# Performance work log

Measured on AMD Instinct MI355X. Metric: run time of the kernel, lower is better.

Reference implementation:

```python
import jax, jax.numpy as jnp
import numpy as np
from jax import lax

N_CLS = 4
ALPHA = 1.0
EPS = 1e-4


def _level_loss(logit, prob_gt, coord_gt, weight_cls):
    # logit: [B, N_cls*A, D, H, W]; prob_gt: [B, A, D, H, W]; coord_gt: [B, K, 4] int
    B, C, D, H, W = logit.shape
    A = C // N_CLS
    logit6 = logit.reshape(B, N_CLS, A, D, H, W)
    prob = jnp.clip(jax.nn.sigmoid(logit6), EPS, 1.0 - EPS)  # [B,N_cls,A,D,H,W]
    prob_max = jnp.max(prob, axis=1)                          # [B,A,D,H,W]

    # --- negative (background) focal term with NMS peak masking ---
    negmask = (prob_gt == -1.0).astype(logit.dtype)
    pooled = lax.reduce_window(prob_max, -jnp.inf, lax.max,
                               (1, 1, 3, 3, 3), (1, 1, 1, 1, 1),
                               [(0, 0), (0, 0), (1, 1), (1, 1), (1, 1)])
    max_filter = lax.stop_gradient((pooled == prob_max).astype(logit.dtype))
    thresh_filter = (prob_max > EPS).astype(logit.dtype)
    negmask = negmask * max_filter * thresh_filter
    w_neg = lax.stop_gradient(prob_max) ** ALPHA * negmask
    loss_neg = -jnp.sum(jnp.log(1.0 - prob_max) * w_neg)
    count_neg = jnp.sum(w_neg)

    # --- positive + other-class terms at sparse GT coordinates (vmapped over batch) ---
    def per_item(p_pred, l_pred, c_gt, p_gt):
        # p_pred/l_pred: [N_cls,A,D,H,W]; c_gt: [K,4]; p_gt: [A,D,H,W]
        valid = c_gt[:, 0] > -1
        vmask = valid.astype(p_pred.dtype)
        c = jnp.where(valid[:, None], c_gt, 0)  # safe indices for padded rows
        a, d, h, w = c[:, 0], c[:, 1], c[:, 2], c[:, 3]
        cls_gt = jnp.clip(p_gt[a, d, h, w].astype(jnp.int32) - 1, 0, N_CLS - 1)  # [K]
        p_t = p_pred[cls_gt, a, d, h, w]  # [K]
        l_t = l_pred[cls_gt, a, d, h, w]
        w_pos = (1.0 - lax.stop_gradient(p_t)) ** ALPHA * weight_cls[cls_gt] * vmask
        loss_pos = -jnp.sum(jax.nn.log_sigmoid(l_t) * w_pos)
        count_pos = jnp.sum(w_pos)
        # other-class suppression
        p_o = p_pred[:, a, d, h, w]  # [N_cls, K]
        l_o = l_pred[:, a, d, h, w]
        w_o = lax.stop_gradient(
            jax.nn.relu(p_o - (p_t - 0.05))
            * (p_o > 0.5).astype(p_o.dtype)
            * (p_t > 0.5).astype(p_o.dtype))
        # torch: weight[cls_gt] = 0  -> zero entire rows for classes present among valid GTs
        present = jnp.zeros((N_CLS,), p_pred.dtype).at[cls_gt].max(vmask)
        w_o = w_o * (1.0 - present)[:, None] * vmask[None, :]
        loss_other = jnp.sum(-jax.nn.log_sigmoid(-l_o) * w_o)
        count_other = jnp.sum(w_o)
        return loss_pos, count_pos, loss_other, count_other

    lp, cp, lo, co = jax.vmap(per_item)(prob, logit6, coord_gt, prob_gt)
    return (jnp.sum(lp), loss_neg, jnp.sum(lo), jnp.sum(cp), count_neg, jnp.sum(co))


def _forward(logits0, logits1, gtprob0, gtprob1, coords0, coords1, weight_cls):
    r0 = _level_loss(logits0, gtprob0, coords0, weight_cls)
    r1 = _level_loss(logits1, gtprob1, coords1, weight_cls)
    # [loss_pos, loss_neg, loss_other, count_pos, count_neg, count_other]
    return jnp.stack([a + b for a, b in zip(r0, r1)])


def setup_inputs() -> dict:
    rng = np.random.default_rng(0)
    B, A = 2, 2
    level_shapes = [(64, 128, 128), (32, 64, 64)]
    K, K_VALID = 32, 24
    out = {}
    for i, (D, H, W) in enumerate(level_shapes):
        logits = rng.standard_normal((B, N_CLS * A, D, H, W)).astype(np.float32)
        gt = -np.ones((B, A, D, H, W), np.float32)
        coords = -np.ones((B, K, 4), np.int32)
        for b in range(B):
            a = rng.integers(0, A, K_VALID)
            d = rng.integers(0, D, K_VALID)
            h = rng.integers(0, H, K_VALID)
            w = rng.integers(0, W, K_VALID)
            cls = rng.integers(1, N_CLS + 1, K_VALID)
            gt[b, a, d, h, w] = cls.astype(np.float32)
            coords[b, :K_VALID, 0] = a
            coords[b, :K_VALID, 1] = d
            coords[b, :K_VALID, 2] = h
            coords[b, :K_VALID, 3] = w
        out[f"logits{i}"] = jnp.asarray(logits)
        out[f"gtprob{i}"] = jnp.asarray(gt)
        out[f"coords{i}"] = jnp.asarray(coords)
    out["weight_cls"] = jnp.ones((N_CLS,), jnp.float32)
    return out


def reference(logits0, logits1, gtprob0, gtprob1, coords0, coords1, weight_cls):
    return _forward(logits0, logits1, gtprob0, gtprob1, coords0, coords1, weight_cls)
```

## Files before the change

kernel.cpp:

```cpp
#include <hip/hip_runtime.h>
#include <math.h>

#define EPSF 1e-4f
#define NBLK 1024

static __device__ __forceinline__ float sigmoid_fast(float x) {
    float e = __expf(-x);
    float p = __builtin_amdgcn_rcpf(1.0f + e);
    return fminf(fmaxf(p, EPSF), 1.0f - EPSF);
}
static __device__ __forceinline__ float sigmoid_precise(float x) {
    float p = 1.0f / (1.0f + expf(-x));
    return fminf(fmaxf(p, EPSF), 1.0f - EPSF);
}
static __device__ __forceinline__ float softplus(float x) {
    return fmaxf(x, 0.0f) + log1pf(expf(-fabsf(x)));
}
static __device__ __forceinline__ float4 fmax4(float4 a, float4 b) {
    float4 r;
    r.x = fmaxf(a.x, b.x); r.y = fmaxf(a.y, b.y);
    r.z = fmaxf(a.z, b.z); r.w = fmaxf(a.w, b.w);
    return r;
}
static __device__ __forceinline__ float4 sig4(float4 x) {
    float4 r;
    r.x = sigmoid_fast(x.x); r.y = sigmoid_fast(x.y);
    r.z = sigmoid_fast(x.z); r.w = sigmoid_fast(x.w);
    return r;
}

template <int WG, int Wc>
static __device__ __forceinline__ float4 wmax_row(const float* pm, int row, int w0) {
    const float4 v = *(const float4*)(pm + (size_t)row * Wc + 4 * w0);
    float lft = __shfl_up(v.w, 1);
    float rgt = __shfl_down(v.x, 1);
    lft = (w0 == 0) ? -INFINITY : lft;
    rgt = (w0 == WG - 1) ? -INFINITY : rgt;
    float4 r;
    r.x = fmaxf(fmaxf(lft, v.x), v.y);
    r.y = fmaxf(fmaxf(v.x, v.y), v.z);
    r.z = fmaxf(fmaxf(v.y, v.z), v.w);
    r.w = fmaxf(fmaxf(v.z, v.w), rgt);
    return r;
}
template <int WG, int Wc>
static __device__ __forceinline__ float4 hfold(const float* pm, int row0, int w0) {
    return fmax4(fmax4(wmax_row<WG, Wc>(pm, row0, w0), wmax_row<WG, Wc>(pm, row0 + 1, w0)),
                 wmax_row<WG, Wc>(pm, row0 + 2, w0));
}

template <int Wc, int TD, int TH>
static __device__ void neg_tile(const float* __restrict__ logits,
                                const float* __restrict__ gtprob,
                                int D, int H, int tileIdx, float* pm,
                                double& lsum, double& csum) {
    constexpr int WG = Wc / 4;
    constexpr int NROWH = TH + 2;
    constexpr int NROW = (TD + 2) * NROWH;
    constexpr int RPP = 512 / WG;
    constexpr int G = 512 / WG;
    const int ht = tileIdx & 15, dt = (tileIdx >> 4) & 15, ab = tileIdx >> 8;
    const int a = ab & 1, b = ab >> 1;
    const int h0 = ht * TH, d0 = dt * TD;
    size_t HW = (size_t)H * Wc;
    size_t vol = (size_t)D * HW;
    const float* lg = logits + ((size_t)b * 8 + a) * vol;
    const size_t cs = 2 * vol;
    const float* gtb = gtprob + ((size_t)b * 2 + a) * vol;
    const int tid = threadIdx.x;
    const int w0 = tid % WG, rg = tid / WG;

#pragma unroll
    for (int r = rg; r < NROW; r += RPP) {
        int rd = r / NROWH, rh = r - rd * NROWH;
        int d = d0 + rd - 1, h = h0 + rh - 1;
        float4 v = make_float4(-INFINITY, -INFINITY, -INFINITY, -INFINITY);
        if ((unsigned)d < (unsigned)D && (unsigned)h < (unsigned)H) {
            const float* p0 = lg + (size_t)d * HW + (size_t)h * Wc + 4 * w0;
            float4 c0 = *(const float4*)(p0);
            float4 c1 = *(const float4*)(p0 + cs);
            float4 c2 = *(const float4*)(p0 + 2 * cs);
            float4 c3 = *(const float4*)(p0 + 3 * cs);
            v = sig4(fmax4(fmax4(c0, c1), fmax4(c2, c3)));
        }
        *(float4*)(pm + (size_t)r * Wc + 4 * w0) = v;
    }
    __syncthreads();

    for (int cidx = rg; cidx < TD * TH; cidx += G) {
        int dd = cidx / TH, hh = cidx - dd * TH;
        float4 hm0 = hfold<WG, Wc>(pm, (dd + 0) * NROWH + hh, w0);
        float4 hm1 = hfold<WG, Wc>(pm, (dd + 1) * NROWH + hh, w0);
        float4 hm2 = hfold<WG, Wc>(pm, (dd + 2) * NROWH + hh, w0);
        float4 mx = fmax4(fmax4(hm0, hm1), hm2);
        float4 pc = *(const float4*)(pm + (size_t)((dd + 1) * NROWH + hh + 1) * Wc + 4 * w0);
        const float* gp = gtb + (size_t)(d0 + dd) * HW + (size_t)(h0 + hh) * Wc + 4 * w0;
        float4 g = *(const float4*)gp;
        if (g.x == -1.0f && mx.x == pc.x && pc.x > EPSF) {
            lsum += (double)(-__logf(1.0f - pc.x) * pc.x); csum += (double)pc.x;
        }
        if (g.y == -1.0f && mx.y == pc.y && pc.y > EPSF) {
            lsum += (double)(-__logf(1.0f - pc.y) * pc.y); csum += (double)pc.y;
        }
        if (g.z == -1.0f && mx.z == pc.z && pc.z > EPSF) {
            lsum += (double)(-__logf(1.0f - pc.z) * pc.z); csum += (double)pc.z;
        }
        if (g.w == -1.0f && mx.w == pc.w && pc.w > EPSF) {
            lsum += (double)(-__logf(1.0f - pc.w) * pc.w); csum += (double)pc.w;
        }
    }
}

__global__ __launch_bounds__(512) void fused_kernel(
    const float* __restrict__ lg0, const float* __restrict__ gt0, const int* __restrict__ c0,
    const float* __restrict__ lg1, const float* __restrict__ gt1, const int* __restrict__ c1,
    const float* __restrict__ wcls, double* __restrict__ slots,
    unsigned* __restrict__ counter, float* __restrict__ out) {
    __shared__ float pm[60 * 128];
    __shared__ double spart[48];
    __shared__ unsigned present[4];
    __shared__ bool isLast;
    int tid = threadIdx.x;
    int bid = blockIdx.x;
    double v0 = 0, v1 = 0, v2 = 0, v3 = 0, v4 = 0, v5 = 0;

    if (bid == 0) {
        if (tid < 4) present[tid] = 0u;
        __syncthreads();
        int lvl = (tid >> 6) & 1, tt = tid & 63;
        int b = tt >> 5, k = tt & 31;
        const float* lg = lvl ? lg1 : lg0;
        const float* gt = lvl ? gt1 : gt0;
        const int* cd = lvl ? c1 : c0;
        int D = lvl ? 32 : 64, H = lvl ? 64 : 128, Wd = lvl ? 64 : 128;
        int a = 0, d = 0, h = 0, w = 0, cls = 0;
        bool valid = false;
        size_t vol = (size_t)D * H * Wd, off = 0;
        if (tid < 128) {
            const int* c = cd + ((size_t)b * 32 + k) * 4;
            a = c[0]; d = c[1]; h = c[2]; w = c[3];
            valid = a > -1;
            if (!valid) { a = 0; d = 0; h = 0; w = 0; }
            off = ((size_t)d * H + h) * (size_t)Wd + w;
            float gval = gt[((size_t)b * 2 + a) * vol + off];
            cls = (int)gval - 1;
            cls = cls < 0 ? 0 : (cls > 3 ? 3 : cls);
            if (valid) atomicOr(&present[lvl * 2 + b], 1u << cls);
        }
        __syncthreads();
        if (tid < 128) {
            unsigned pmask = present[lvl * 2 + b];
            float vm = valid ? 1.0f : 0.0f;
            const float* lgb = lg + (size_t)b * 8 * vol;
            size_t aoff = (size_t)a * vol + off;
            float l_t = lgb[(size_t)cls * 2 * vol + aoff];
            float p_t = sigmoid_precise(l_t);
            float w_pos = (1.0f - p_t) * wcls[cls] * vm;
            float loss_pos = softplus(-l_t) * w_pos;
            float ptg = (p_t > 0.5f) ? 1.0f : 0.0f;
            float lo = 0.0f, co = 0.0f;
#pragma unroll
            for (int cc = 0; cc < 4; cc++) {
                float l_o = lgb[(size_t)cc * 2 * vol + aoff];
                float p_o = sigmoid_precise(l_o);
                float wo = fmaxf(p_o - (p_t - 0.05f), 0.0f) * ((p_o > 0.5f) ? 1.0f : 0.0f) * ptg;
                float pres = ((pmask >> cc) & 1u) ? 1.0f : 0.0f;
                wo *= (1.0f - pres) * vm;
                lo += softplus(l_o) * wo;
                co += wo;
            }
            v0 = loss_pos; v3 = w_pos; v2 = lo; v5 = co;
        }
        __syncthreads();
    }

    neg_tile<128, 4, 8>(lg0, gt0, 64, 128, bid, pm, v1, v4);
    __syncthreads();
    neg_tile<64, 2, 4>(lg1, gt1, 32, 64, bid, pm, v1, v4);

    for (int o = 32; o > 0; o >>= 1) {
        v0 += __shfl_down(v0, o); v1 += __shfl_down(v1, o); v2 += __shfl_down(v2, o);
        v3 += __shfl_down(v3, o); v4 += __shfl_down(v4, o); v5 += __shfl_down(v5, o);
    }
    int wave = tid >> 6, lane = tid & 63;
    if (lane == 0) {
        double* sp = spart + wave * 6;
        sp[0] = v0; sp[1] = v1; sp[2] = v2; sp[3] = v3; sp[4] = v4; sp[5] = v5;
    }
    __syncthreads();
    if (tid == 0) {
        double s[6] = {0, 0, 0, 0, 0, 0};
#pragma unroll
        for (int wv = 0; wv < 8; wv++)
#pragma unroll
            for (int j = 0; j < 6; j++) s[j] += spart[wv * 6 + j];
        double* slot = slots + (size_t)bid * 6;
#pragma unroll
        for (int j = 0; j < 6; j++) slot[j] = s[j];
        __threadfence();
        unsigned prev = atomicAdd(counter, 1u);
        isLast = (prev == NBLK - 1);
    }
    __syncthreads();
    if (isLast) {
        __threadfence();
        double acc[6] = {0, 0, 0, 0, 0, 0};
        for (int i = tid; i < NBLK; i += 512) {
            const double* sl = slots + (size_t)i * 6;
#pragma unroll
            for (int j = 0; j < 6; j++) acc[j] += sl[j];
        }
#pragma unroll
        for (int j = 0; j < 6; j++)
            for (int o = 32; o > 0; o >>= 1) acc[j] += __shfl_down(acc[j], o);
        __syncthreads();
        if (lane == 0) {
            double* sp = spart + wave * 6;
#pragma unroll
            for (int j = 0; j < 6; j++) sp[j] = acc[j];
        }
        __syncthreads();
        if (tid == 0) {
#pragma unroll
            for (int j = 0; j < 6; j++) {
                double s = 0;
#pragma unroll
                for (int wv = 0; wv < 8; wv++) s += spart[wv * 6 + j];
                out[j] = (float)s;
            }
        }
    }
}

extern "C" void kernel_launch(void* const* d_in, const int* in_sizes, int n_in,
                              void* d_out, int out_size, void* d_ws, size_t ws_size,
                              hipStream_t stream) {
    const float *logits0 = nullptr, *gtprob0 = nullptr, *logits1 = nullptr,
                *gtprob1 = nullptr, *wcls = nullptr;
    const int *coords0 = nullptr, *coords1 = nullptr;
    for (int i = 0; i < n_in; i++) {
        switch (in_sizes[i]) {
            case 16777216: logits0 = (const float*)d_in[i]; break;
            case 4194304:  gtprob0 = (const float*)d_in[i]; break;
            case 2097152:  logits1 = (const float*)d_in[i]; break;
            case 524288:   gtprob1 = (const float*)d_in[i]; break;
            case 4:        wcls    = (const float*)d_in[i]; break;
            case 256:
                if (!coords0) coords0 = (const int*)d_in[i];
                else          coords1 = (const int*)d_in[i];
                break;
        }
    }
    unsigned* counter = (unsigned*)d_ws;
    double* slots = (double*)((char*)d_ws + 64);
    hipMemsetAsync(d_ws, 0, 64, stream);
    fused_kernel<<<NBLK, 512, 0, stream>>>(logits0, gtprob0, coords0,
                                           logits1, gtprob1, coords1,
                                           wcls, slots, counter, (float*)d_out);
}
```

Before: 163.7 us.

## Split levels across separate block ranges, prefetch rows, use global atomics

Each block now handles a single level's tile: 1024 blocks take level 0 and 128 blocks take level 1 with larger tiles, so a block no longer runs both levels back to back. The halo-row loader is software-pipelined, fetching the next row's four class loads before computing the current one, and ground-truth loads are hoisted ahead of the barrier. The last-block slot reduction is replaced with double atomicAdd into six global accumulators plus a tiny finalize kernel. This adds a second launch and double atomics, and makes the summation order nondeterministic.

```diff
diff --git a/kernel.cpp b/kernel.cpp
--- a/kernel.cpp
+++ b/kernel.cpp
@@ -2,7 +2,9 @@
 #include <math.h>
 
 #define EPSF 1e-4f
-#define NBLK 1024
+#define NB_L1 128
+#define NB_L0 1024
+#define NBLK (NB_L1 + NB_L0)
 
 static __device__ __forceinline__ float sigmoid_fast(float x) {
     float e = __expf(-x);
@@ -49,53 +51,90 @@
                  wmax_row<WG, Wc>(pm, row0 + 2, w0));
 }
 
-template <int Wc, int TD, int TH>
+template <int Wc, int TD, int TH, int D, int H>
 static __device__ void neg_tile(const float* __restrict__ logits,
                                 const float* __restrict__ gtprob,
-                                int D, int H, int tileIdx, float* pm,
+                                int tileIdx, float* pm,
                                 double& lsum, double& csum) {
     constexpr int WG = Wc / 4;
     constexpr int NROWH = TH + 2;
     constexpr int NROW = (TD + 2) * NROWH;
     constexpr int RPP = 512 / WG;
-    constexpr int G = 512 / WG;
-    const int ht = tileIdx & 15, dt = (tileIdx >> 4) & 15, ab = tileIdx >> 8;
+    constexpr int NPASS = (NROW + RPP - 1) / RPP;
+    constexpr int NCELL = TD * TH;
+    constexpr int CPT = (NCELL + RPP - 1) / RPP;
+    constexpr int NH = H / TH, ND = D / TD;
+    const int ht = tileIdx % NH;
+    const int dt = (tileIdx / NH) % ND;
+    const int ab = tileIdx / (NH * ND);
     const int a = ab & 1, b = ab >> 1;
     const int h0 = ht * TH, d0 = dt * TD;
-    size_t HW = (size_t)H * Wc;
-    size_t vol = (size_t)D * HW;
+    const size_t HW = (size_t)H * Wc;
+    const size_t vol = (size_t)D * HW;
     const float* lg = logits + ((size_t)b * 8 + a) * vol;
     const size_t cs = 2 * vol;
     const float* gtb = gtprob + ((size_t)b * 2 + a) * vol;
     const int tid = threadIdx.x;
     const int w0 = tid % WG, rg = tid / WG;
 
-#pragma unroll
-    for (int r = rg; r < NROW; r += RPP) {
-        int rd = r / NROWH, rh = r - rd * NROWH;
+    auto rowinfo = [&](int r, bool& inb) -> const float* {
+        int rc = r < NROW - 1 ? r : NROW - 1;
+        int rd = rc / NROWH, rh = rc - rd * NROWH;
         int d = d0 + rd - 1, h = h0 + rh - 1;
-        float4 v = make_float4(-INFINITY, -INFINITY, -INFINITY, -INFINITY);
-        if ((unsigned)d < (unsigned)D && (unsigned)h < (unsigned)H) {
-            const float* p0 = lg + (size_t)d * HW + (size_t)h * Wc + 4 * w0;
-            float4 c0 = *(const float4*)(p0);
-            float4 c1 = *(const float4*)(p0 + cs);
-            float4 c2 = *(const float4*)(p0 + 2 * cs);
-            float4 c3 = *(const float4*)(p0 + 3 * cs);
-            v = sig4(fmax4(fmax4(c0, c1), fmax4(c2, c3)));
-        }
-        *(float4*)(pm + (size_t)r * Wc + 4 * w0) = v;
+        inb = ((unsigned)d < (unsigned)D) & ((unsigned)h < (unsigned)H) & (r < NROW);
+        int dc = d < 0 ? 0 : (d >= D ? D - 1 : d);
+        int hc = h < 0 ? 0 : (h >= H ? H - 1 : h);
+        return lg + (size_t)dc * HW + (size_t)hc * Wc + 4 * w0;
+    };
+
+    float4 n0, n1, n2, n3;
+    bool ninb;
+    {
+        const float* p = rowinfo(rg, ninb);
+        n0 = *(const float4*)p;            n1 = *(const float4*)(p + cs);
+        n2 = *(const float4*)(p + 2 * cs); n3 = *(const float4*)(p + 3 * cs);
+    }
+#pragma unroll
+    for (int ps = 0; ps < NPASS; ps++) {
+        float4 c0 = n0, c1 = n1, c2 = n2, c3 = n3;
+        bool inb = ninb;
+        int r = rg + ps * RPP;
+        if (ps + 1 < NPASS) {
+            bool ib;
+            const float* q = rowinfo(rg + (ps + 1) * RPP, ib);
+            ninb = ib;
+            n0 = *(const float4*)q;            n1 = *(const float4*)(q + cs);
+            n2 = *(const float4*)(q + 2 * cs); n3 = *(const float4*)(q + 3 * cs);
+        }
+        float4 v = sig4(fmax4(fmax4(c0, c1), fmax4(c2, c3)));
+        if (!inb) v = make_float4(-INFINITY, -INFINITY, -INFINITY, -INFINITY);
+        if (r < NROW) *(float4*)(pm + (size_t)r * Wc + 4 * w0) = v;
+    }
+
+    float4 gq[CPT];
+    int cdd[CPT], chh[CPT];
+    bool cok[CPT];
+#pragma unroll
+    for (int k = 0; k < CPT; k++) {
+        int cidx = rg + k * RPP;
+        bool ok = cidx < NCELL;
+        int ci = ok ? cidx : 0;
+        int dd = ci / TH, hh = ci - dd * TH;
+        cdd[k] = dd; chh[k] = hh; cok[k] = ok;
+        gq[k] = *(const float4*)(gtb + (size_t)(d0 + dd) * HW + (size_t)(h0 + hh) * Wc + 4 * w0);
     }
     __syncthreads();
 
-    for (int cidx = rg; cidx < TD * TH; cidx += G) {
-        int dd = cidx / TH, hh = cidx - dd * TH;
+#pragma unroll
+    for (int k = 0; k < CPT; k++) {
+        if (!cok[k]) continue;
+        int dd = cdd[k], hh = chh[k];
         float4 hm0 = hfold<WG, Wc>(pm, (dd + 0) * NROWH + hh, w0);
         float4 hm1 = hfold<WG, Wc>(pm, (dd + 1) * NROWH + hh, w0);
         float4 hm2 = hfold<WG, Wc>(pm, (dd + 2) * NROWH + hh, w0);
         float4 mx = fmax4(fmax4(hm0, hm1), hm2);
         float4 pc = *(const float4*)(pm + (size_t)((dd + 1) * NROWH + hh + 1) * Wc + 4 * w0);
-        const float* gp = gtb + (size_t)(d0 + dd) * HW + (size_t)(h0 + hh) * Wc + 4 * w0;
-        float4 g = *(const float4*)gp;
+        float4 g = gq[k];
         if (g.x == -1.0f && mx.x == pc.x && pc.x > EPSF) {
             lsum += (double)(-__logf(1.0f - pc.x) * pc.x); csum += (double)pc.x;
         }
@@ -114,73 +153,78 @@
 __global__ __launch_bounds__(512) void fused_kernel(
     const float* __restrict__ lg0, const float* __restrict__ gt0, const int* __restrict__ c0,
     const float* __restrict__ lg1, const float* __restrict__ gt1, const int* __restrict__ c1,
-    const float* __restrict__ wcls, double* __restrict__ slots,
-    unsigned* __restrict__ counter, float* __restrict__ out) {
+    const float* __restrict__ wcls, double* __restrict__ gacc) {
     __shared__ float pm[60 * 128];
     __shared__ double spart[48];
     __shared__ unsigned present[4];
-    __shared__ bool isLast;
     int tid = threadIdx.x;
     int bid = blockIdx.x;
     double v0 = 0, v1 = 0, v2 = 0, v3 = 0, v4 = 0, v5 = 0;
 
+    if (bid >= NB_L1) {
+        neg_tile<128, 4, 8, 64, 128>(lg0, gt0, bid - NB_L1, pm, v1, v4);
+    } else {
+        if (bid == 0) {
+            if (tid < 4) present[tid] = 0u;
+            __syncthreads();
+            int lvl = (tid >> 6) & 1, tt = tid & 63;
+            int b = tt >> 5, k = tt & 31;
+            const float* lg = lvl ? lg1 : lg0;
+            const float* gt = lvl ? gt1 : gt0;
+            const int* cd = lvl ? c1 : c0;
+            int D = lvl ? 32 : 64, H = lvl ? 64 : 128, Wd = lvl ? 64 : 128;
+            int a = 0, d = 0, h = 0, w = 0, cls = 0;
+            bool valid = false;
+            size_t vol = (size_t)D * H * Wd, off = 0;
+            if (tid < 128) {
+                const int* c = cd + ((size_t)b * 32 + k) * 4;
+                a = c[0]; d = c[1]; h = c[2]; w = c[3];
+                valid = a > -1;
+                if (!valid) { a = 0; d = 0; h = 0; w = 0; }
+                off = ((size_t)d * H + h) * (size_t)Wd + w;
+                float gval = gt[((size_t)b * 2 + a) * vol + off];
+                cls = (int)gval - 1;
+                cls = cls < 0 ? 0 : (cls > 3 ? 3 : cls);
+                if (valid) atomicOr(&present[lvl * 2 + b], 1u << cls);
+            }
+            __syncthreads();
+            if (tid < 128) {
+                unsigned pmask = present[lvl * 2 + b];
+                float vm = valid ? 1.0f : 0.0f;
+                const float* lgb = lg + (size_t)b * 8 * vol;
+                size_t aoff = (size_t)a * vol + off;
+                float l_t = lgb[(size_t)cls * 2 * vol + aoff];
+                float p_t = sigmoid_precise(l_t);
+                float w_pos = (1.0f - p_t) * wcls[cls] * vm;
+                float loss_pos = softplus(-l_t) * w_pos;
+                float ptg = (p_t > 0.5f) ? 1.0f : 0.0f;
+                float lo = 0.0f, co = 0.0f;
+#pragma unroll
+                for (int cc = 0; cc < 4; cc++) {
+                    float l_o = lgb[(size_t)cc * 2 * vol + aoff];
+                    float p_o = sigmoid_precise(l_o);
+                    float wo = fmaxf(p_o - (p_t - 0.05f), 0.0f) * ((p_o > 0.5f) ? 1.0f : 0.0f) * ptg;
+                    float pres = ((pmask >> cc) & 1u) ? 1.0f : 0.0f;
+                    wo *= (1.0f - pres) * vm;
+                    lo += softplus(l_o) * wo;
+                    co += wo;
+                }
+                v0 = loss_pos; v3 = w_pos; v2 = lo; v5 = co;
+            }
+            __syncthreads();
+        }
+        neg_tile<64, 8, 8, 32, 64>(lg1, gt1, bid, pm, v1, v4);
+    }
+
+    for (int o = 32; o > 0; o >>= 1) {
+        v1 += __shfl_down(v1, o);
+        v4 += __shfl_down(v4, o);
+    }
     if (bid == 0) {
-        if (tid < 4) present[tid] = 0u;
-        __syncthreads();
-        int lvl = (tid >> 6) & 1, tt = tid & 63;
-        int b = tt >> 5, k = tt & 31;
-        const float* lg = lvl ? lg1 : lg0;
-        const float* gt = lvl ? gt1 : gt0;
-        const int* cd = lvl ? c1 : c0;
-        int D = lvl ? 32 : 64, H = lvl ? 64 : 128, Wd = lvl ? 64 : 128;
-        int a = 0, d = 0, h = 0, w = 0, cls = 0;
-        bool valid = false;
-        size_t vol = (size_t)D * H * Wd, off = 0;
-        if (tid < 128) {
-            const int* c = cd + ((size_t)b * 32 + k) * 4;
-            a = c[0]; d = c[1]; h = c[2]; w = c[3];
-            valid = a > -1;
-            if (!valid) { a = 0; d = 0; h = 0; w = 0; }
-            off = ((size_t)d * H + h) * (size_t)Wd + w;
-            float gval = gt[((size_t)b * 2 + a) * vol + off];
-            cls = (int)gval - 1;
-            cls = cls < 0 ? 0 : (cls > 3 ? 3 : cls);
-            if (valid) atomicOr(&present[lvl * 2 + b], 1u << cls);
-        }
-        __syncthreads();
-        if (tid < 128) {
-            unsigned pmask = present[lvl * 2 + b];
-            float vm = valid ? 1.0f : 0.0f;
-            const float* lgb = lg + (size_t)b * 8 * vol;
-            size_t aoff = (size_t)a * vol + off;
-            float l_t = lgb[(size_t)cls * 2 * vol + aoff];
-            float p_t = sigmoid_precise(l_t);
-            float w_pos = (1.0f - p_t) * wcls[cls] * vm;
-            float loss_pos = softplus(-l_t) * w_pos;
-            float ptg = (p_t > 0.5f) ? 1.0f : 0.0f;
-            float lo = 0.0f, co = 0.0f;
-#pragma unroll
-            for (int cc = 0; cc < 4; cc++) {
-                float l_o = lgb[(size_t)cc * 2 * vol + aoff];
-                float p_o = sigmoid_precise(l_o);
-                float wo = fmaxf(p_o - (p_t - 0.05f), 0.0f) * ((p_o > 0.5f) ? 1.0f : 0.0f) * ptg;
-                float pres = ((pmask >> cc) & 1u) ? 1.0f : 0.0f;
-                wo *= (1.0f - pres) * vm;
-                lo += softplus(l_o) * wo;
-                co += wo;
-            }
-            v0 = loss_pos; v3 = w_pos; v2 = lo; v5 = co;
-        }
-        __syncthreads();
-    }
-
-    neg_tile<128, 4, 8>(lg0, gt0, 64, 128, bid, pm, v1, v4);
-    __syncthreads();
-    neg_tile<64, 2, 4>(lg1, gt1, 32, 64, bid, pm, v1, v4);
-
-    for (int o = 32; o > 0; o >>= 1) {
-        v0 += __shfl_down(v0, o); v1 += __shfl_down(v1, o); v2 += __shfl_down(v2, o);
-        v3 += __shfl_down(v3, o); v4 += __shfl_down(v4, o); v5 += __shfl_down(v5, o);
+        for (int o = 32; o > 0; o >>= 1) {
+            v0 += __shfl_down(v0, o); v2 += __shfl_down(v2, o);
+            v3 += __shfl_down(v3, o); v5 += __shfl_down(v5, o);
+        }
     }
     int wave = tid >> 6, lane = tid & 63;
     if (lane == 0) {
@@ -189,47 +233,27 @@
     }
     __syncthreads();
     if (tid == 0) {
-        double s[6] = {0, 0, 0, 0, 0, 0};
-#pragma unroll
-        for (int wv = 0; wv < 8; wv++)
-#pragma unroll
-            for (int j = 0; j < 6; j++) s[j] += spart[wv * 6 + j];
-        double* slot = slots + (size_t)bid * 6;
-#pragma unroll
-        for (int j = 0; j < 6; j++) slot[j] = s[j];
-        __threadfence();
-        unsigned prev = atomicAdd(counter, 1u);
-        isLast = (prev == NBLK - 1);
-    }
-    __syncthreads();
-    if (isLast) {
-        __threadfence();
-        double acc[6] = {0, 0, 0, 0, 0, 0};
-        for (int i = tid; i < NBLK; i += 512) {
-            const double* sl = slots + (size_t)i * 6;
-#pragma unroll
-            for (int j = 0; j < 6; j++) acc[j] += sl[j];
-        }
-#pragma unroll
-        for (int j = 0; j < 6; j++)
-            for (int o = 32; o > 0; o >>= 1) acc[j] += __shfl_down(acc[j], o);
-        __syncthreads();
-        if (lane == 0) {
-            double* sp = spart + wave * 6;
-#pragma unroll
-            for (int j = 0; j < 6; j++) sp[j] = acc[j];
-        }
-        __syncthreads();
-        if (tid == 0) {
-#pragma unroll
-            for (int j = 0; j < 6; j++) {
-                double s = 0;
-#pragma unroll
-                for (int wv = 0; wv < 8; wv++) s += spart[wv * 6 + j];
-                out[j] = (float)s;
+        double s1 = 0, s4 = 0;
+#pragma unroll
+        for (int wv = 0; wv < 8; wv++) { s1 += spart[wv * 6 + 1]; s4 += spart[wv * 6 + 4]; }
+        atomicAdd(&gacc[1], s1);
+        atomicAdd(&gacc[4], s4);
+        if (bid == 0) {
+            double s0 = 0, s2 = 0, s3 = 0, s5 = 0;
+#pragma unroll
+            for (int wv = 0; wv < 8; wv++) {
+                s0 += spart[wv * 6 + 0]; s2 += spart[wv * 6 + 2];
+                s3 += spart[wv * 6 + 3]; s5 += spart[wv * 6 + 5];
             }
-        }
-    }
+            atomicAdd(&gacc[0], s0); atomicAdd(&gacc[2], s2);
+            atomicAdd(&gacc[3], s3); atomicAdd(&gacc[5], s5);
+        }
+    }
+}
+
+__global__ void finalize_kernel(const double* __restrict__ gacc, float* __restrict__ out) {
+    int i = threadIdx.x;
+    if (i < 6) out[i] = (float)gacc[i];
 }
 
 extern "C" void kernel_launch(void* const* d_in, const int* in_sizes, int n_in,
@@ -251,10 +275,10 @@
                 break;
         }
     }
-    unsigned* counter = (unsigned*)d_ws;
-    double* slots = (double*)((char*)d_ws + 64);
-    hipMemsetAsync(d_ws, 0, 64, stream);
+    double* gacc = (double*)d_ws;
+    hipMemsetAsync(d_ws, 0, 6 * sizeof(double), stream);
     fused_kernel<<<NBLK, 512, 0, stream>>>(logits0, gtprob0, coords0,
                                            logits1, gtprob1, coords1,
-                                           wcls, slots, counter, (float*)d_out);
-}
+                                           wcls, gacc);
+    finalize_kernel<<<1, 64, 0, stream>>>(gacc, (float*)d_out);
+}
```

Result: faster. 146.8 us (-10.3%).
